# Kernel optimization log

Hardware: AMD Instinct MI355X
Metric: run time of the kernel (lower is better)

Reference implementation:

```python
import jax, jax.numpy as jnp
import numpy as np


def setup_inputs() -> dict:
    key = jax.random.key(0)
    k1, k2, k3, k4 = jax.random.split(key, 4)
    B, N, L, H, E = 2, 128, 128, 8, 64
    queries = jax.random.normal(k1, (B, N, L, H, E), dtype=jnp.float32)
    keys = jax.random.normal(k2, (B, N, L, H, E), dtype=jnp.float32)
    values = jax.random.normal(k3, (B, N, L, H, E), dtype=jnp.float32)
    # multiplicative spatial adjacency mask [B, N, M]
    attn_mask = jax.random.uniform(k4, (B, N, N), dtype=jnp.float32)
    return {"queries": queries, "keys": keys, "values": values, "attn_mask": attn_mask}


def reference(queries, keys, values, attn_mask):
    # queries/keys/values: [B, N, L, H, E]; attn_mask: [B, N, M]
    E = queries.shape[-1]
    scale = 1.0 / jnp.sqrt(jnp.asarray(E, queries.dtype))
    # --- temporal attention (per node, over time L) ---
    scores_t = jnp.einsum('bnlhe,bnshe->bnhls', queries, keys)  # [B,N,H,L,S]
    A_t = jax.nn.softmax(scale * scores_t, axis=-1)
    # dropout is identity at inference (Keras default training=False)
    V_t = jnp.einsum('bnhls,bnshd->bnlhd', A_t, values)  # [B,N,L,H,D]
    # --- spatial attention (per timestep, over nodes N) ---
    scores_s = jnp.einsum('bnlhe,bmlhe->blhnm', queries, keys)  # [B,L,H,N,M]
    scores_s = scores_s * attn_mask[:, None, None, :, :]        # multiplicative adjacency mask
    A_s = jax.nn.softmax(scale * scores_s, axis=-1)
    V = jnp.einsum('blhnm,bmlhd->bnlhd', A_s, V_t)  # [B,N,L,H,D]
    return V
```

## Files before the change

### kernel.cpp

```cpp
#include <hip/hip_runtime.h>

static constexpr int Bb = 2, Nn = 128, Ll = 128, Hh = 8, Ee = 64;
static constexpr float SCALE = 0.125f;

typedef short short8 __attribute__((ext_vector_type(8)));
typedef float float4v __attribute__((ext_vector_type(4)));

#define MFMA16(a, b, c) __builtin_amdgcn_mfma_f32_16x16x32_bf16(a, b, c, 0, 0, 0)

__device__ inline unsigned short bf16_rne(float f) {
  unsigned u = __builtin_bit_cast(unsigned, f);
  u += 0x7FFFu + ((u >> 16) & 1u);
  return (unsigned short)(u >> 16);
}

__device__ inline void split8(float4 a, float4 b, short8& hi, short8& lo) {
  float f[8] = {a.x, a.y, a.z, a.w, b.x, b.y, b.z, b.w};
#pragma unroll
  for (int j = 0; j < 8; ++j) {
    unsigned u = __builtin_bit_cast(unsigned, f[j]);
    unsigned short h = (unsigned short)(u >> 16);
    hi[j] = (short)h;
    float hf = __builtin_bit_cast(float, (unsigned)h << 16);
    lo[j] = (short)bf16_rne(f[j] - hf);
  }
}

__device__ inline short8 pack4(const unsigned* p) {
  union { unsigned u[4]; short8 s; } t;
  t.u[0] = p[0]; t.u[1] = p[1]; t.u[2] = p[2]; t.u[3] = p[3];
  return t.s;
}

__global__ __launch_bounds__(256, 3) void st_attn(
    const float* __restrict__ Qp, const float* __restrict__ Kp,
    const float* __restrict__ Vp, const float* __restrict__ Mp,
    float* __restrict__ Op, int idx_stride, int row_stride) {
  __shared__ __align__(16) unsigned short Pb[128 * 130];
  __shared__ __align__(16) unsigned short Vb[64 * 130];

  const int g = blockIdx.x;
  const int b = g >> 10;
  const int idx = (g >> 3) & 127;
  const int h = g & 7;
  const int base = b * (Nn * Ll * Hh * Ee) + idx * idx_stride + h * Ee;

  const int tid = threadIdx.x;
  const int wave = tid >> 6;
  const int lane = tid & 63;
  const int tx = lane & 15;
  const int quad = lane >> 4;

#pragma unroll
  for (int it = 0; it < 8; ++it) {
    const int i4 = tid + it * 256;
    const int c = i4 >> 4;
    const int d0 = (i4 & 15) << 2;
    const float4 v = *(const float4*)(Vp + base + c * row_stride + d0);
    Vb[(d0 + 0) * 130 + c] = bf16_rne(v.x);
    Vb[(d0 + 1) * 130 + c] = bf16_rne(v.y);
    Vb[(d0 + 2) * 130 + c] = bf16_rne(v.z);
    Vb[(d0 + 3) * 130 + c] = bf16_rne(v.w);
  }

  short8 qhi[2][2], qlo[2][2];
#pragma unroll
  for (int rt = 0; rt < 2; ++rt) {
    const float* qr = Qp + base + (wave * 32 + rt * 16 + tx) * row_stride;
#pragma unroll
    for (int ks = 0; ks < 2; ++ks) {
      const float4 a = *(const float4*)(qr + ks * 32 + quad * 8);
      const float4 c = *(const float4*)(qr + ks * 32 + quad * 8 + 4);
      split8(a, c, qhi[rt][ks], qlo[rt][ks]);
    }
  }

  float4v acc[2][8];
#pragma unroll
  for (int rt = 0; rt < 2; ++rt)
#pragma unroll
    for (int ct = 0; ct < 8; ++ct) acc[rt][ct] = (float4v)(0.0f);

#pragma unroll
  for (int ct = 0; ct < 8; ++ct) {
    const float* kr = Kp + base + (ct * 16 + tx) * row_stride;
#pragma unroll
    for (int ks = 0; ks < 2; ++ks) {
      const float4 a = *(const float4*)(kr + ks * 32 + quad * 8);
      const float4 c = *(const float4*)(kr + ks * 32 + quad * 8 + 4);
      short8 khi, klo;
      split8(a, c, khi, klo);
#pragma unroll
      for (int rt = 0; rt < 2; ++rt) {
        acc[rt][ct] = MFMA16(qhi[rt][ks], khi, acc[rt][ct]);
        acc[rt][ct] = MFMA16(qhi[rt][ks], klo, acc[rt][ct]);
        acc[rt][ct] = MFMA16(qlo[rt][ks], khi, acc[rt][ct]);
      }
    }
  }

  const bool has_mask = (Mp != nullptr);
  const int mb = b * (Nn * Nn);
  float rowsum[2][4];
#pragma unroll
  for (int rt = 0; rt < 2; ++rt)
#pragma unroll
    for (int e = 0; e < 4; ++e) rowsum[rt][e] = 0.f;

#pragma unroll
  for (int rt = 0; rt < 2; ++rt) {
    const int rowb = wave * 32 + rt * 16 + quad * 4;
#pragma unroll
    for (int ct = 0; ct < 8; ++ct) {
      const int col = ct * 16 + tx;
      float mv[4];
      if (has_mask) {
#pragma unroll
        for (int e = 0; e < 4; ++e) mv[e] = Mp[mb + (rowb + e) * 128 + col];
      }
#pragma unroll
      for (int e = 0; e < 4; ++e) {
        float p = acc[rt][ct][e] * SCALE;
        if (has_mask) p *= mv[e];
        p = __expf(p);
        rowsum[rt][e] += p;
        Pb[(rowb + e) * 130 + col] = bf16_rne(p);
      }
    }
  }

  float inv[2][4];
#pragma unroll
  for (int rt = 0; rt < 2; ++rt)
#pragma unroll
    for (int e = 0; e < 4; ++e) {
      float s = rowsum[rt][e];
#pragma unroll
      for (int d = 1; d < 16; d <<= 1) s += __shfl_xor(s, d);
      inv[rt][e] = 1.0f / s;
    }

  __syncthreads();

  float4v accO[2][4];
#pragma unroll
  for (int rt = 0; rt < 2; ++rt)
#pragma unroll
    for (int dt = 0; dt < 4; ++dt) accO[rt][dt] = (float4v)(0.0f);

#pragma unroll
  for (int ks = 0; ks < 4; ++ks) {
    short8 pA[2];
#pragma unroll
    for (int rt = 0; rt < 2; ++rt) {
      const unsigned* pw = (const unsigned*)Pb +
                           (wave * 32 + rt * 16 + tx) * 65 + ks * 16 + quad * 4;
      pA[rt] = pack4(pw);
    }
#pragma unroll
    for (int dt = 0; dt < 4; ++dt) {
      const unsigned* vw =
          (const unsigned*)Vb + (dt * 16 + tx) * 65 + ks * 16 + quad * 4;
      const short8 vB = pack4(vw);
      accO[0][dt] = MFMA16(pA[0], vB, accO[0][dt]);
      accO[1][dt] = MFMA16(pA[1], vB, accO[1][dt]);
    }
  }

#pragma unroll
  for (int rt = 0; rt < 2; ++rt) {
    const int rowb = wave * 32 + rt * 16 + quad * 4;
#pragma unroll
    for (int dt = 0; dt < 4; ++dt) {
#pragma unroll
      for (int e = 0; e < 4; ++e) {
        Op[base + (rowb + e) * row_stride + dt * 16 + tx] =
            accO[rt][dt][e] * inv[rt][e];
      }
    }
  }
}

extern "C" void kernel_launch(void* const* d_in, const int* in_sizes, int n_in,
                              void* d_out, int out_size, void* d_ws,
                              size_t ws_size, hipStream_t stream) {
  const float* Q = (const float*)d_in[0];
  const float* K = (const float*)d_in[1];
  const float* V = (const float*)d_in[2];
  const float* M = (const float*)d_in[3];
  float* out = (float*)d_out;
  float* Vt = (float*)d_ws;

  dim3 grid(Bb * Nn * Hh), blk(256);
  st_attn<<<grid, blk, 0, stream>>>(Q, K, V, nullptr, Vt,
                                    Ll * Hh * Ee ,
                                    Hh * Ee );
  st_attn<<<grid, blk, 0, stream>>>(Q, K, Vt, M, out, Hh * Ee ,
                                    Ll * Hh * Ee );
}
```

Before: 303.7 us.

## Stage K tile in shared memory as pre-split bf16 hi/lo with XOR swizzle

K rows are now loaded once per block with coalesced float4 reads, split into bf16 hi/lo, and stored in the P buffer using an XOR-swizzled layout. The QK MFMA loop then reads the K fragments from LDS instead of having every wave reload and re-split K from global memory. This removes the four-fold redundant global K traffic and split work across waves. In exchange it adds two extra block barriers, and the exponentiated scores must stay in registers until K is no longer needed, which raises register pressure.

```diff
diff --git a/kernel.cpp b/kernel.cpp
--- a/kernel.cpp
+++ b/kernel.cpp
@@ -4,6 +4,7 @@
 static constexpr float SCALE = 0.125f;
 
 typedef short short8 __attribute__((ext_vector_type(8)));
+typedef short short4v __attribute__((ext_vector_type(4)));
 typedef float float4v __attribute__((ext_vector_type(4)));
 
 #define MFMA16(a, b, c) __builtin_amdgcn_mfma_f32_16x16x32_bf16(a, b, c, 0, 0, 0)
@@ -12,6 +13,18 @@
   unsigned u = __builtin_bit_cast(unsigned, f);
   u += 0x7FFFu + ((u >> 16) & 1u);
   return (unsigned short)(u >> 16);
+}
+
+__device__ inline void split4(float4 a, short4v& hi, short4v& lo) {
+  float f[4] = {a.x, a.y, a.z, a.w};
+#pragma unroll
+  for (int j = 0; j < 4; ++j) {
+    unsigned u = __builtin_bit_cast(unsigned, f[j]);
+    unsigned short h = (unsigned short)(u >> 16);
+    hi[j] = (short)h;
+    float hf = __builtin_bit_cast(float, (unsigned)h << 16);
+    lo[j] = (short)bf16_rne(f[j] - hf);
+  }
 }
 
 __device__ inline void split8(float4 a, float4 b, short8& hi, short8& lo) {
@@ -63,6 +76,21 @@
     Vb[(d0 + 3) * 130 + c] = bf16_rne(v.w);
   }
 
+#pragma unroll
+  for (int it = 0; it < 8; ++it) {
+    const int i4 = tid + it * 256;
+    const int r = i4 >> 4;
+    const int d0 = (i4 & 15) << 2;
+    const float4 kv = *(const float4*)(Kp + base + r * row_stride + d0);
+    const int vs = d0 >> 3;
+    const int idxk =
+        ((((r >> 4) * 8 + vs) * 16 + (r & 15)) ^ vs) * 8 + (d0 & 7);
+    short4v h4, l4;
+    split4(kv, h4, l4);
+    *(short4v*)(Pb + idxk) = h4;
+    *(short4v*)(Pb + idxk + 8192) = l4;
+  }
+
   short8 qhi[2][2], qlo[2][2];
 #pragma unroll
   for (int rt = 0; rt < 2; ++rt) {
@@ -75,21 +103,23 @@
     }
   }
 
+  __syncthreads();
+
   float4v acc[2][8];
 #pragma unroll
   for (int rt = 0; rt < 2; ++rt)
 #pragma unroll
     for (int ct = 0; ct < 8; ++ct) acc[rt][ct] = (float4v)(0.0f);
 
+  const short8* KS8 = (const short8*)Pb;
 #pragma unroll
   for (int ct = 0; ct < 8; ++ct) {
-    const float* kr = Kp + base + (ct * 16 + tx) * row_stride;
 #pragma unroll
     for (int ks = 0; ks < 2; ++ks) {
-      const float4 a = *(const float4*)(kr + ks * 32 + quad * 8);
-      const float4 c = *(const float4*)(kr + ks * 32 + quad * 8 + 4);
-      short8 khi, klo;
-      split8(a, c, khi, klo);
+      const int vs = ks * 4 + quad;
+      const int fi = (((ct * 8 + vs) * 16 + tx) ^ vs);
+      const short8 khi = KS8[fi];
+      const short8 klo = KS8[fi + 1024];
 #pragma unroll
       for (int rt = 0; rt < 2; ++rt) {
         acc[rt][ct] = MFMA16(qhi[rt][ks], khi, acc[rt][ct]);
@@ -124,7 +154,7 @@
         if (has_mask) p *= mv[e];
         p = __expf(p);
         rowsum[rt][e] += p;
-        Pb[(rowb + e) * 130 + col] = bf16_rne(p);
+        acc[rt][ct][e] = p;
       }
     }
   }
@@ -139,6 +169,20 @@
       for (int d = 1; d < 16; d <<= 1) s += __shfl_xor(s, d);
       inv[rt][e] = 1.0f / s;
     }
+
+  __syncthreads();
+
+#pragma unroll
+  for (int rt = 0; rt < 2; ++rt) {
+    const int rowb = wave * 32 + rt * 16 + quad * 4;
+#pragma unroll
+    for (int ct = 0; ct < 8; ++ct) {
+      const int col = ct * 16 + tx;
+#pragma unroll
+      for (int e = 0; e < 4; ++e)
+        Pb[(rowb + e) * 130 + col] = bf16_rne(acc[rt][ct][e]);
+    }
+  }
 
   __syncthreads();
 
```

After: 284.6 us. 1.07x faster.
